# Optimization experiments

Measured on AMD Instinct MI355X. Metric: run time of the kernel, lower is better.

Reference implementation:

```python
import jax, jax.numpy as jnp
import numpy as np

B, N, K = 16, 16384, 32

def _fit_motion_svd_batch(pc1, pc2, m):
    # pc1, pc2: (BK, N, 3); m: (BK, N) soft weights
    w_sum = jnp.sum(m, axis=1, keepdims=True)                      # (BK,1)
    pc1_mean = jnp.einsum('bnd,bn->bd', pc1, m) / w_sum            # (BK,3)
    pc2_mean = jnp.einsum('bnd,bn->bd', pc2, m) / w_sum
    pc1_c = pc1 - pc1_mean[:, None, :]
    pc2_c = pc2 - pc2_mean[:, None, :]
    # S = pc1_c^T diag(m) pc2_c : (BK,3,3)
    S = jnp.einsum('bnd,bn,bne->bde', pc1_c, m, pc2_c)
    invalid = jnp.any(jnp.isnan(S), axis=(1, 2))                   # (BK,)
    S_safe = jnp.where(invalid[:, None, None], jnp.eye(3, dtype=S.dtype), S)
    u, s, vh = jnp.linalg.svd(S_safe, full_matrices=True)
    v = jnp.swapaxes(vh, -1, -2)
    R0 = jnp.einsum('bij,bkj->bik', v, u)                          # v @ u^T
    det = jnp.linalg.det(R0)
    diag = jnp.stack([jnp.ones_like(det), jnp.ones_like(det), det], axis=-1)
    R = jnp.einsum('bij,bj,bkj->bik', v, diag, u)                  # v diag u^T
    t = pc2_mean - jnp.einsum('bij,bj->bi', R, pc1_mean)
    R = jnp.where(invalid[:, None, None], jnp.eye(3, dtype=R.dtype), R)
    t = jnp.where(invalid[:, None], jnp.zeros_like(t), t)
    return R, t

def setup_inputs() -> dict:
    key = jax.random.key(0)
    k1, k2, k3 = jax.random.split(key, 3)
    pc = jax.random.normal(k1, (B, N, 3), dtype=jnp.float32)
    mask = jax.random.uniform(k2, (B, N, K), dtype=jnp.float32)
    flow = jax.random.normal(k3, (B, N, 3), dtype=jnp.float32)
    return {"pc": pc, "mask": mask, "flow": flow}

def reference(pc, mask, flow):
    loss_norm = 2
    n_batch, n_point, n_object = mask.shape
    pc2 = pc + flow                                                # (B,N,3)
    m = jnp.swapaxes(mask, 1, 2).reshape(n_batch * n_object, n_point)
    pc_rep = jnp.broadcast_to(pc[:, None], (n_batch, n_object, n_point, 3)).reshape(-1, n_point, 3)
    pc2_rep = jnp.broadcast_to(pc2[:, None], (n_batch, n_object, n_point, 3)).reshape(-1, n_point, 3)
    # pc_transformed is detached in the original; detach inputs to the fit (equivalent)
    R, t = _fit_motion_svd_batch(jax.lax.stop_gradient(pc_rep),
                                 jax.lax.stop_gradient(pc2_rep),
                                 jax.lax.stop_gradient(m))
    pc_tr = jnp.einsum('bij,bnj->bni', R, jax.lax.stop_gradient(pc_rep)) + t[:, None, :]
    pc_tr = pc_tr.reshape(n_batch, n_object, n_point, 3)           # already grad-free
    m4 = m.reshape(n_batch, n_object, n_point)[..., None]          # (B,K,N,1), carries grad
    pc_blend = jnp.sum(m4 * pc_tr, axis=1)                         # (B,N,3)
    diff = pc_blend - pc2
    loss = jnp.linalg.norm(diff, ord=loss_norm, axis=-1)
    return jnp.mean(loss)
```

## Files before the change

### kernel.cpp

```cpp
#include <hip/hip_runtime.h>
#include <math.h>

#define BB 16
#define NPTS 16384
#define KK 32

#define CHUNK1 512
#define NCHUNK1 (NPTS / CHUNK1)

__global__ __launch_bounds__(256) void phase1_kernel(
    const float* __restrict__ pc, const float* __restrict__ mask,
    const float* __restrict__ flow, float* __restrict__ p1) {
  const int b = blockIdx.y;
  const int chunk = blockIdx.x;
  const int tid = threadIdx.x;
  const int plane = tid >> 5;

  const float* pcb = pc + (size_t)b * NPTS * 3;
  const float* flb = flow + (size_t)b * NPTS * 3;
  const size_t mbase = ((size_t)b * NPTS + (size_t)chunk * CHUNK1) * KK;

  float w = 0.f;
  float ax = 0.f, ay = 0.f, az = 0.f;
  float bx = 0.f, by = 0.f, bz = 0.f;
  float M00 = 0.f, M01 = 0.f, M02 = 0.f;
  float M10 = 0.f, M11 = 0.f, M12 = 0.f;
  float M20 = 0.f, M21 = 0.f, M22 = 0.f;

  const int base_p = chunk * CHUNK1 + plane;
#pragma unroll 4
  for (int i = 0; i < CHUNK1 / 8; ++i) {
    const int p = base_p + i * 8;
    const float m = mask[mbase + (size_t)i * 256 + tid];
    const float px = pcb[p * 3 + 0];
    const float py = pcb[p * 3 + 1];
    const float pz = pcb[p * 3 + 2];
    const float qx = px + flb[p * 3 + 0];
    const float qy = py + flb[p * 3 + 1];
    const float qz = pz + flb[p * 3 + 2];
    w += m;
    const float mx = m * px, my = m * py, mz = m * pz;
    ax += mx; ay += my; az += mz;
    bx = fmaf(m, qx, bx); by = fmaf(m, qy, by); bz = fmaf(m, qz, bz);
    M00 = fmaf(mx, qx, M00); M01 = fmaf(mx, qy, M01); M02 = fmaf(mx, qz, M02);
    M10 = fmaf(my, qx, M10); M11 = fmaf(my, qy, M11); M12 = fmaf(my, qz, M12);
    M20 = fmaf(mz, qx, M20); M21 = fmaf(mz, qy, M21); M22 = fmaf(mz, qz, M22);
  }

  __shared__ float red[256][17];
  red[tid][0] = w;
  red[tid][1] = ax; red[tid][2] = ay; red[tid][3] = az;
  red[tid][4] = bx; red[tid][5] = by; red[tid][6] = bz;
  red[tid][7] = M00; red[tid][8] = M01; red[tid][9] = M02;
  red[tid][10] = M10; red[tid][11] = M11; red[tid][12] = M12;
  red[tid][13] = M20; red[tid][14] = M21; red[tid][15] = M22;
  __syncthreads();

  if (tid < 32) {
    float s[16];
#pragma unroll
    for (int v = 0; v < 16; ++v) s[v] = 0.f;
#pragma unroll
    for (int pl = 0; pl < 8; ++pl) {
#pragma unroll
      for (int v = 0; v < 16; ++v) s[v] += red[pl * 32 + tid][v];
    }
    float* dst = p1 + (((size_t)b * NCHUNK1 + chunk) * 32 + tid) * 16;
#pragma unroll
    for (int v = 0; v < 16; ++v) dst[v] = s[v];
  }
}

__global__ void phase2_kernel(const float* __restrict__ p1,
                              float* __restrict__ rt) {
  const int idx = blockIdx.x * blockDim.x + threadIdx.x;
  if (idx >= BB * KK) return;
  const int b = idx >> 5, k = idx & 31;

  double s[16];
#pragma unroll
  for (int v = 0; v < 16; ++v) s[v] = 0.0;
  for (int c = 0; c < NCHUNK1; ++c) {
    const float* src = p1 + (((size_t)b * NCHUNK1 + c) * 32 + k) * 16;
#pragma unroll
    for (int v = 0; v < 16; ++v) s[v] += (double)src[v];
  }

  const double w = s[0];
  const double mu1[3] = {s[1] / w, s[2] / w, s[3] / w};
  const double bs[3] = {s[4], s[5], s[6]};
  const double mu2[3] = {bs[0] / w, bs[1] / w, bs[2] / w};

  double S[3][3];
#pragma unroll
  for (int d = 0; d < 3; ++d)
#pragma unroll
    for (int e = 0; e < 3; ++e) S[d][e] = s[7 + d * 3 + e] - mu1[d] * bs[e];

  double A[3][3];
#pragma unroll
  for (int i = 0; i < 3; ++i)
#pragma unroll
    for (int j = 0; j < 3; ++j)
      A[i][j] = S[0][i] * S[0][j] + S[1][i] * S[1][j] + S[2][i] * S[2][j];

  double V[3][3] = {{1, 0, 0}, {0, 1, 0}, {0, 0, 1}};

  for (int sweep = 0; sweep < 8; ++sweep) {
#pragma unroll
    for (int pair = 0; pair < 3; ++pair) {
      const int p = (pair == 0) ? 0 : (pair == 1) ? 0 : 1;
      const int q = (pair == 0) ? 1 : (pair == 1) ? 2 : 2;
      const double apq = A[p][q];
      if (fabs(apq) < 1e-300) continue;
      const double app = A[p][p], aqq = A[q][q];
      const double tau = (aqq - app) / (2.0 * apq);
      const double tt =
          ((tau >= 0.0) ? 1.0 : -1.0) / (fabs(tau) + sqrt(1.0 + tau * tau));
      const double c = 1.0 / sqrt(1.0 + tt * tt);
      const double sn = tt * c;
      const int r = 3 - p - q;
      const double arp = A[r][p], arq = A[r][q];
      A[r][p] = A[p][r] = c * arp - sn * arq;
      A[r][q] = A[q][r] = sn * arp + c * arq;
      A[p][p] = app - tt * apq;
      A[q][q] = aqq + tt * apq;
      A[p][q] = A[q][p] = 0.0;
#pragma unroll
      for (int i = 0; i < 3; ++i) {
        const double vip = V[i][p], viq = V[i][q];
        V[i][p] = c * vip - sn * viq;
        V[i][q] = sn * vip + c * viq;
      }
    }
  }

  int id0 = 0, id1 = 1, id2 = 2;
  double lam[3] = {A[0][0], A[1][1], A[2][2]};
  if (lam[id0] < lam[id1]) { int t = id0; id0 = id1; id1 = t; }
  if (lam[id0] < lam[id2]) { int t = id0; id0 = id2; id2 = t; }
  if (lam[id1] < lam[id2]) { int t = id1; id1 = id2; id2 = t; }
  const int ord[3] = {id0, id1, id2};

  double Vs[3][3], U[3][3];
#pragma unroll
  for (int j = 0; j < 3; ++j) {
    const int cj = ord[j];
    const double lj = lam[cj] > 0.0 ? lam[cj] : 0.0;
    const double sig = sqrt(lj);
    const double inv = 1.0 / (sig > 1e-30 ? sig : 1e-30);
#pragma unroll
    for (int i = 0; i < 3; ++i) Vs[i][j] = V[i][cj];
#pragma unroll
    for (int i = 0; i < 3; ++i)
      U[i][j] =
          (S[i][0] * Vs[0][j] + S[i][1] * Vs[1][j] + S[i][2] * Vs[2][j]) * inv;
  }

  const double detS = S[0][0] * (S[1][1] * S[2][2] - S[1][2] * S[2][1]) -
                      S[0][1] * (S[1][0] * S[2][2] - S[1][2] * S[2][0]) +
                      S[0][2] * (S[1][0] * S[2][1] - S[1][1] * S[2][0]);
  const double sgn = (detS >= 0.0) ? 1.0 : -1.0;

  double R[3][3];
#pragma unroll
  for (int i = 0; i < 3; ++i)
#pragma unroll
    for (int j = 0; j < 3; ++j)
      R[i][j] = Vs[i][0] * U[j][0] + Vs[i][1] * U[j][1] + sgn * Vs[i][2] * U[j][2];

  double tv[3];
#pragma unroll
  for (int i = 0; i < 3; ++i)
    tv[i] = mu2[i] - (R[i][0] * mu1[0] + R[i][1] * mu1[1] + R[i][2] * mu1[2]);

  float* dst = rt + (size_t)idx * 12;
#pragma unroll
  for (int i = 0; i < 3; ++i)
#pragma unroll
    for (int j = 0; j < 3; ++j) dst[i * 3 + j] = (float)R[i][j];
#pragma unroll
  for (int i = 0; i < 3; ++i) dst[9 + i] = (float)tv[i];
}

#define PTS3 256
#define NCHUNK3 (NPTS / PTS3)

__global__ __launch_bounds__(256) void phase3_kernel(
    const float* __restrict__ pc, const float* __restrict__ mask,
    const float* __restrict__ flow, const float* __restrict__ rt,
    float* __restrict__ p3) {
  const int b = blockIdx.y;
  const int chunk = blockIdx.x;
  const int tid = threadIdx.x;

  __shared__ float4 sR[KK * 3];
  for (int l = tid; l < KK * 3; l += 256)
    sR[l] = ((const float4*)rt)[(size_t)b * KK * 3 + l];
  __syncthreads();

  const int p = chunk * PTS3 + tid;
  const float4* mrow = (const float4*)(mask + ((size_t)b * NPTS + p) * KK);
  float4 mv[8];
#pragma unroll
  for (int j = 0; j < 8; ++j) mv[j] = mrow[j];

  const float* pcp = pc + ((size_t)b * NPTS + p) * 3;
  const float* flp = flow + ((size_t)b * NPTS + p) * 3;
  const float px = pcp[0], py = pcp[1], pz = pcp[2];

  float C[12];
#pragma unroll
  for (int v = 0; v < 12; ++v) C[v] = 0.f;

#pragma unroll
  for (int k = 0; k < KK; ++k) {
    const float m = ((const float*)&mv[k >> 2])[k & 3];
    const float4 r0 = sR[k * 3 + 0];
    const float4 r1 = sR[k * 3 + 1];
    const float4 r2 = sR[k * 3 + 2];
    C[0] = fmaf(m, r0.x, C[0]); C[1] = fmaf(m, r0.y, C[1]);
    C[2] = fmaf(m, r0.z, C[2]); C[3] = fmaf(m, r0.w, C[3]);
    C[4] = fmaf(m, r1.x, C[4]); C[5] = fmaf(m, r1.y, C[5]);
    C[6] = fmaf(m, r1.z, C[6]); C[7] = fmaf(m, r1.w, C[7]);
    C[8] = fmaf(m, r2.x, C[8]); C[9] = fmaf(m, r2.y, C[9]);
    C[10] = fmaf(m, r2.z, C[10]); C[11] = fmaf(m, r2.w, C[11]);
  }

  const float vx = fmaf(C[0], px, fmaf(C[1], py, fmaf(C[2], pz, C[9])));
  const float vy = fmaf(C[3], px, fmaf(C[4], py, fmaf(C[5], pz, C[10])));
  const float vz = fmaf(C[6], px, fmaf(C[7], py, fmaf(C[8], pz, C[11])));

  const float qx = px + flp[0];
  const float qy = py + flp[1];
  const float qz = pz + flp[2];
  const float dx = vx - qx, dy = vy - qy, dz = vz - qz;
  float acc = sqrtf(dx * dx + dy * dy + dz * dz);

#pragma unroll
  for (int off = 32; off >= 1; off >>= 1) acc += __shfl_xor(acc, off, 64);
  __shared__ float sred[4];
  if ((tid & 63) == 0) sred[tid >> 6] = acc;
  __syncthreads();
  if (tid == 0)
    p3[(size_t)b * NCHUNK3 + chunk] = sred[0] + sred[1] + sred[2] + sred[3];
}

__global__ void phase4_kernel(const float* __restrict__ p3,
                              float* __restrict__ out) {
  const int tid = threadIdx.x;
  float v = 0.f;
#pragma unroll
  for (int j = 0; j < 4; ++j) v += p3[j * 256 + tid];
#pragma unroll
  for (int off = 32; off >= 1; off >>= 1) v += __shfl_xor(v, off, 64);
  __shared__ float sr[4];
  if ((tid & 63) == 0) sr[tid >> 6] = v;
  __syncthreads();
  if (tid == 0)
    out[0] = (sr[0] + sr[1] + sr[2] + sr[3]) * (1.0f / ((float)BB * NPTS));
}

extern "C" void kernel_launch(void* const* d_in, const int* in_sizes, int n_in,
                              void* d_out, int out_size, void* d_ws,
                              size_t ws_size, hipStream_t stream) {
  const float* pc = (const float*)d_in[0];
  const float* mask = (const float*)d_in[1];
  const float* flow = (const float*)d_in[2];
  float* out = (float*)d_out;
  float* ws = (float*)d_ws;

  float* rt = ws;
  float* p1 = ws + 6144;
  float* p3 = ws + 6144 + (size_t)BB * NCHUNK1 * 32 * 16;

  phase1_kernel<<<dim3(NCHUNK1, BB), 256, 0, stream>>>(pc, mask, flow, p1);
  phase2_kernel<<<2, 256, 0, stream>>>(p1, rt);
  phase3_kernel<<<dim3(NCHUNK3, BB), 256, 0, stream>>>(pc, mask, flow, rt, p3);
  phase4_kernel<<<1, 256, 0, stream>>>(p3, out);
}
```

Measured before the change: 113.5 us.

## Parallelize partial-moment reduction across 512 threads per batch before SVD solve

Replaces the serial per-(batch,object) partial reduction in phase 2 with a per-batch block of 512 threads. Each thread sums one moment component over all chunks with coalesced loads, stages the result in shared memory, and then 32 threads run the 3x3 SVD solve. It also halves the phase-1 chunk size to launch more blocks, raises the unroll, and cuts Jacobi sweeps from 8 to 6. The risk is more partial data to reduce and slightly less eigen-solver convergence margin.

```diff
diff --git a/kernel.cpp b/kernel.cpp
--- a/kernel.cpp
+++ b/kernel.cpp
@@ -5,7 +5,7 @@
 #define NPTS 16384
 #define KK 32
 
-#define CHUNK1 512
+#define CHUNK1 256
 #define NCHUNK1 (NPTS / CHUNK1)
 
 __global__ __launch_bounds__(256) void phase1_kernel(
@@ -28,7 +28,7 @@
   float M20 = 0.f, M21 = 0.f, M22 = 0.f;
 
   const int base_p = chunk * CHUNK1 + plane;
-#pragma unroll 4
+#pragma unroll 8
   for (int i = 0; i < CHUNK1 / 8; ++i) {
     const int p = base_p + i * 8;
     const float m = mask[mbase + (size_t)i * 256 + tid];
@@ -71,116 +71,122 @@
   }
 }
 
-__global__ void phase2_kernel(const float* __restrict__ p1,
-                              float* __restrict__ rt) {
-  const int idx = blockIdx.x * blockDim.x + threadIdx.x;
-  if (idx >= BB * KK) return;
-  const int b = idx >> 5, k = idx & 31;
-
-  double s[16];
-#pragma unroll
-  for (int v = 0; v < 16; ++v) s[v] = 0.0;
-  for (int c = 0; c < NCHUNK1; ++c) {
-    const float* src = p1 + (((size_t)b * NCHUNK1 + c) * 32 + k) * 16;
-#pragma unroll
-    for (int v = 0; v < 16; ++v) s[v] += (double)src[v];
-  }
-
-  const double w = s[0];
-  const double mu1[3] = {s[1] / w, s[2] / w, s[3] / w};
-  const double bs[3] = {s[4], s[5], s[6]};
-  const double mu2[3] = {bs[0] / w, bs[1] / w, bs[2] / w};
-
-  double S[3][3];
-#pragma unroll
-  for (int d = 0; d < 3; ++d)
-#pragma unroll
-    for (int e = 0; e < 3; ++e) S[d][e] = s[7 + d * 3 + e] - mu1[d] * bs[e];
-
-  double A[3][3];
-#pragma unroll
-  for (int i = 0; i < 3; ++i)
-#pragma unroll
-    for (int j = 0; j < 3; ++j)
-      A[i][j] = S[0][i] * S[0][j] + S[1][i] * S[1][j] + S[2][i] * S[2][j];
-
-  double V[3][3] = {{1, 0, 0}, {0, 1, 0}, {0, 0, 1}};
-
-  for (int sweep = 0; sweep < 8; ++sweep) {
-#pragma unroll
-    for (int pair = 0; pair < 3; ++pair) {
-      const int p = (pair == 0) ? 0 : (pair == 1) ? 0 : 1;
-      const int q = (pair == 0) ? 1 : (pair == 1) ? 2 : 2;
-      const double apq = A[p][q];
-      if (fabs(apq) < 1e-300) continue;
-      const double app = A[p][p], aqq = A[q][q];
-      const double tau = (aqq - app) / (2.0 * apq);
-      const double tt =
-          ((tau >= 0.0) ? 1.0 : -1.0) / (fabs(tau) + sqrt(1.0 + tau * tau));
-      const double c = 1.0 / sqrt(1.0 + tt * tt);
-      const double sn = tt * c;
-      const int r = 3 - p - q;
-      const double arp = A[r][p], arq = A[r][q];
-      A[r][p] = A[p][r] = c * arp - sn * arq;
-      A[r][q] = A[q][r] = sn * arp + c * arq;
-      A[p][p] = app - tt * apq;
-      A[q][q] = aqq + tt * apq;
-      A[p][q] = A[q][p] = 0.0;
-#pragma unroll
-      for (int i = 0; i < 3; ++i) {
-        const double vip = V[i][p], viq = V[i][q];
-        V[i][p] = c * vip - sn * viq;
-        V[i][q] = sn * vip + c * viq;
+__global__ __launch_bounds__(512) void solve_kernel(
+    const float* __restrict__ p1, float* __restrict__ rt) {
+  const int b = blockIdx.x;
+  const int tid = threadIdx.x;
+
+  const float* src = p1 + (size_t)b * (NCHUNK1 * 512) + tid;
+  double acc = 0.0;
+#pragma unroll 8
+  for (int c = 0; c < NCHUNK1; ++c) acc += (double)src[(size_t)c * 512];
+  __shared__ double smom[512];
+  smom[tid] = acc;
+  __syncthreads();
+
+  if (tid < 32) {
+    const int k = tid;
+    double s[16];
+#pragma unroll
+    for (int v = 0; v < 16; ++v) s[v] = smom[k * 16 + v];
+
+    const double w = s[0];
+    const double mu1[3] = {s[1] / w, s[2] / w, s[3] / w};
+    const double bs[3] = {s[4], s[5], s[6]};
+    const double mu2[3] = {bs[0] / w, bs[1] / w, bs[2] / w};
+
+    double S[3][3];
+#pragma unroll
+    for (int d = 0; d < 3; ++d)
+#pragma unroll
+      for (int e = 0; e < 3; ++e) S[d][e] = s[7 + d * 3 + e] - mu1[d] * bs[e];
+
+    double A[3][3];
+#pragma unroll
+    for (int i = 0; i < 3; ++i)
+#pragma unroll
+      for (int j = 0; j < 3; ++j)
+        A[i][j] = S[0][i] * S[0][j] + S[1][i] * S[1][j] + S[2][i] * S[2][j];
+
+    double V[3][3] = {{1, 0, 0}, {0, 1, 0}, {0, 0, 1}};
+
+    for (int sweep = 0; sweep < 6; ++sweep) {
+#pragma unroll
+      for (int pair = 0; pair < 3; ++pair) {
+        const int p = (pair == 0) ? 0 : (pair == 1) ? 0 : 1;
+        const int q = (pair == 0) ? 1 : (pair == 1) ? 2 : 2;
+        const double apq = A[p][q];
+        if (fabs(apq) < 1e-300) continue;
+        const double app = A[p][p], aqq = A[q][q];
+        const double tau = (aqq - app) / (2.0 * apq);
+        const double tt =
+            ((tau >= 0.0) ? 1.0 : -1.0) / (fabs(tau) + sqrt(1.0 + tau * tau));
+        const double c = 1.0 / sqrt(1.0 + tt * tt);
+        const double sn = tt * c;
+        const int r = 3 - p - q;
+        const double arp = A[r][p], arq = A[r][q];
+        A[r][p] = A[p][r] = c * arp - sn * arq;
+        A[r][q] = A[q][r] = sn * arp + c * arq;
+        A[p][p] = app - tt * apq;
+        A[q][q] = aqq + tt * apq;
+        A[p][q] = A[q][p] = 0.0;
+#pragma unroll
+        for (int i = 0; i < 3; ++i) {
+          const double vip = V[i][p], viq = V[i][q];
+          V[i][p] = c * vip - sn * viq;
+          V[i][q] = sn * vip + c * viq;
+        }
       }
     }
-  }
-
-  int id0 = 0, id1 = 1, id2 = 2;
-  double lam[3] = {A[0][0], A[1][1], A[2][2]};
-  if (lam[id0] < lam[id1]) { int t = id0; id0 = id1; id1 = t; }
-  if (lam[id0] < lam[id2]) { int t = id0; id0 = id2; id2 = t; }
-  if (lam[id1] < lam[id2]) { int t = id1; id1 = id2; id2 = t; }
-  const int ord[3] = {id0, id1, id2};
-
-  double Vs[3][3], U[3][3];
-#pragma unroll
-  for (int j = 0; j < 3; ++j) {
-    const int cj = ord[j];
-    const double lj = lam[cj] > 0.0 ? lam[cj] : 0.0;
-    const double sig = sqrt(lj);
-    const double inv = 1.0 / (sig > 1e-30 ? sig : 1e-30);
-#pragma unroll
-    for (int i = 0; i < 3; ++i) Vs[i][j] = V[i][cj];
-#pragma unroll
-    for (int i = 0; i < 3; ++i)
-      U[i][j] =
-          (S[i][0] * Vs[0][j] + S[i][1] * Vs[1][j] + S[i][2] * Vs[2][j]) * inv;
-  }
-
-  const double detS = S[0][0] * (S[1][1] * S[2][2] - S[1][2] * S[2][1]) -
-                      S[0][1] * (S[1][0] * S[2][2] - S[1][2] * S[2][0]) +
-                      S[0][2] * (S[1][0] * S[2][1] - S[1][1] * S[2][0]);
-  const double sgn = (detS >= 0.0) ? 1.0 : -1.0;
-
-  double R[3][3];
-#pragma unroll
-  for (int i = 0; i < 3; ++i)
-#pragma unroll
-    for (int j = 0; j < 3; ++j)
-      R[i][j] = Vs[i][0] * U[j][0] + Vs[i][1] * U[j][1] + sgn * Vs[i][2] * U[j][2];
-
-  double tv[3];
-#pragma unroll
-  for (int i = 0; i < 3; ++i)
-    tv[i] = mu2[i] - (R[i][0] * mu1[0] + R[i][1] * mu1[1] + R[i][2] * mu1[2]);
-
-  float* dst = rt + (size_t)idx * 12;
-#pragma unroll
-  for (int i = 0; i < 3; ++i)
-#pragma unroll
-    for (int j = 0; j < 3; ++j) dst[i * 3 + j] = (float)R[i][j];
-#pragma unroll
-  for (int i = 0; i < 3; ++i) dst[9 + i] = (float)tv[i];
+
+    int id0 = 0, id1 = 1, id2 = 2;
+    double lam[3] = {A[0][0], A[1][1], A[2][2]};
+    if (lam[id0] < lam[id1]) { int t = id0; id0 = id1; id1 = t; }
+    if (lam[id0] < lam[id2]) { int t = id0; id0 = id2; id2 = t; }
+    if (lam[id1] < lam[id2]) { int t = id1; id1 = id2; id2 = t; }
+    const int ord[3] = {id0, id1, id2};
+
+    double Vs[3][3], U[3][3];
+#pragma unroll
+    for (int j = 0; j < 3; ++j) {
+      const int cj = ord[j];
+      const double lj = lam[cj] > 0.0 ? lam[cj] : 0.0;
+      const double sig = sqrt(lj);
+      const double inv = 1.0 / (sig > 1e-30 ? sig : 1e-30);
+#pragma unroll
+      for (int i = 0; i < 3; ++i) Vs[i][j] = V[i][cj];
+#pragma unroll
+      for (int i = 0; i < 3; ++i)
+        U[i][j] =
+            (S[i][0] * Vs[0][j] + S[i][1] * Vs[1][j] + S[i][2] * Vs[2][j]) * inv;
+    }
+
+    const double detS = S[0][0] * (S[1][1] * S[2][2] - S[1][2] * S[2][1]) -
+                        S[0][1] * (S[1][0] * S[2][2] - S[1][2] * S[2][0]) +
+                        S[0][2] * (S[1][0] * S[2][1] - S[1][1] * S[2][0]);
+    const double sgn = (detS >= 0.0) ? 1.0 : -1.0;
+
+    double R[3][3];
+#pragma unroll
+    for (int i = 0; i < 3; ++i)
+#pragma unroll
+      for (int j = 0; j < 3; ++j)
+        R[i][j] =
+            Vs[i][0] * U[j][0] + Vs[i][1] * U[j][1] + sgn * Vs[i][2] * U[j][2];
+
+    double tv[3];
+#pragma unroll
+    for (int i = 0; i < 3; ++i)
+      tv[i] = mu2[i] - (R[i][0] * mu1[0] + R[i][1] * mu1[1] + R[i][2] * mu1[2]);
+
+    float* dst = rt + ((size_t)b * KK + k) * 12;
+#pragma unroll
+    for (int i = 0; i < 3; ++i)
+#pragma unroll
+      for (int j = 0; j < 3; ++j) dst[i * 3 + j] = (float)R[i][j];
+#pragma unroll
+    for (int i = 0; i < 3; ++i) dst[9 + i] = (float)tv[i];
+  }
 }
 
 #define PTS3 256
@@ -272,10 +278,10 @@
 
   float* rt = ws;
   float* p1 = ws + 6144;
-  float* p3 = ws + 6144 + (size_t)BB * NCHUNK1 * 32 * 16;
+  float* p3 = p1 + (size_t)BB * NCHUNK1 * 512;
 
   phase1_kernel<<<dim3(NCHUNK1, BB), 256, 0, stream>>>(pc, mask, flow, p1);
-  phase2_kernel<<<2, 256, 0, stream>>>(p1, rt);
+  solve_kernel<<<BB, 512, 0, stream>>>(p1, rt);
   phase3_kernel<<<dim3(NCHUNK3, BB), 256, 0, stream>>>(pc, mask, flow, rt, p3);
   phase4_kernel<<<1, 256, 0, stream>>>(p3, out);
 }
```

New measurement: 118.1 us, median of 2. +4.1%, slower.
